# Optimization experiments

Measured on AMD Instinct MI355X. Metric: run time of the kernel, lower is better.

The kernel has to match this reference:

```python
import jax, jax.numpy as jnp
import numpy as np

N_QUBITS = 5
N_A = 1
N_LAYERS = 4
PATCH = 2 ** (N_QUBITS - N_A)  # 16

CNOT4 = jnp.array([[1, 0, 0, 0], [0, 1, 0, 0], [0, 0, 0, 1], [0, 0, 1, 0]], dtype=jnp.complex64)


def _ry(t):
    c = jnp.cos(t / 2).astype(jnp.complex64)
    s = jnp.sin(t / 2).astype(jnp.complex64)
    return jnp.stack([jnp.stack([c, -s]), jnp.stack([s, c])])


def _rot(phi, theta, omega):
    # PennyLane Rot = RZ(omega) RY(theta) RZ(phi)
    c = jnp.cos(theta / 2)
    s = jnp.sin(theta / 2)
    ep = jnp.exp(-0.5j * (phi + omega))  # e^{-i(phi+omega)/2}
    em = jnp.exp(-0.5j * (phi - omega))  # e^{-i(phi-omega)/2}
    return jnp.stack([jnp.stack([ep * c, -jnp.conj(em) * s]),
                      jnp.stack([em * s, jnp.conj(ep) * c])])


def _apply_1q(state, U, w):
    # contract U onto qubit axis w of state [2]*5
    s = jnp.tensordot(U, state, axes=(1, w))
    return jnp.moveaxis(s, 0, w)


def _apply_cnot(state, c, t):
    perm = jnp.moveaxis(state, (c, t), (0, 1))
    shp = perm.shape
    out = (CNOT4 @ perm.reshape(4, -1)).reshape(shp)
    return jnp.moveaxis(out, (0, 1), (c, t))


def _simulate(noise, w):
    # noise: [5], w: [4,5,3] -> normalized probs over first 16 basis states
    state = jnp.zeros((2,) * N_QUBITS, jnp.complex64).at[(0,) * N_QUBITS].set(1.0)
    for q in range(N_QUBITS):
        state = _apply_1q(state, _ry(noise[q]), q)
    for l in range(N_LAYERS):
        r = l % (N_QUBITS - 1) + 1  # StronglyEntanglingLayers default ranges
        for q in range(N_QUBITS):
            state = _apply_1q(state, _rot(w[l, q, 0], w[l, q, 1], w[l, q, 2]), q)
        for q in range(N_QUBITS):
            state = _apply_cnot(state, q, (q + r) % N_QUBITS)
    probs = jnp.abs(state.reshape(-1)) ** 2  # [32]
    p0 = probs[:PATCH] / jnp.sum(probs)  # partial measure: ancilla wire 4 == 0
    return p0 / jnp.max(p0)


def setup_inputs() -> dict:
    key = jax.random.key(0)
    k1, k2 = jax.random.split(key)
    B, G = 65536, 4
    x = jax.random.uniform(k1, (B, N_QUBITS), dtype=jnp.float32)
    weights = jax.random.uniform(k2, (G, N_LAYERS, N_QUBITS, 3), dtype=jnp.float32)  # q_delta=1
    return {"x": x, "weights": weights}


def reference(x, weights):
    sim_g = jax.vmap(_simulate, in_axes=(None, 0))   # over generators
    sim_bg = jax.vmap(sim_g, in_axes=(0, None))      # over batch
    out = sim_bg(x, weights)                         # [B, G, 16]
    return out.reshape(x.shape[0], -1).astype(jnp.float32)  # [B, G*16]
```

## Files before the change

kernel.cpp:

```cpp
#include <hip/hip_runtime.h>


#define NGEN 4
#define NLAY 4
#define NQ   5

typedef _Float16 half8 __attribute__((ext_vector_type(8)));
typedef float    f32x4 __attribute__((ext_vector_type(4)));

__global__ __launch_bounds__(256) void pqg_precompute(
    const float* __restrict__ w, _Float16* __restrict__ wsA)
{
    __shared__ float gm[NLAY * NQ * 8];
    __shared__ float Sr[32 * 32];
    __shared__ float Si[32 * 32];

    const int g = blockIdx.x;
    const int t = threadIdx.x;

    if (t < NLAY * NQ) {
        const float* wp = w + (g * (NLAY * NQ) + t) * 3;
        const float phi = wp[0], theta = wp[1], omega = wp[2];
        const float a = 0.5f * (phi + omega);
        const float bb = 0.5f * (phi - omega);
        const float h = 0.5f * theta;
        const float sa = __sinf(a), ca = __cosf(a);
        const float sb = __sinf(bb), cb = __cosf(bb);
        const float st = __sinf(h), ct = __cosf(h);
        float* m = &gm[t * 8];
        m[0] =  ca * ct;  m[1] = -sa * ct;
        m[2] = -cb * st;  m[3] = -sb * st;
        m[4] =  cb * st;  m[5] = -sb * st;
        m[6] =  ca * ct;  m[7] =  sa * ct;
    }

#pragma unroll
    for (int r = 0; r < 4; ++r) {
        const int idx = r * 256 + t;
        Sr[idx] = ((idx >> 5) == (idx & 31)) ? 1.0f : 0.0f;
        Si[idx] = 0.0f;
    }
    __syncthreads();

    const int col = t & 31;
    const int p0  = t >> 5;

    int gate = 0;
#pragma clang loop unroll(disable)
    for (int l = 0; l < NLAY; ++l) {
#pragma clang loop unroll(disable)
        for (int q = 0; q < NQ; ++q, ++gate) {
            const float* m = &gm[gate * 8];
            const float u00r = m[0], u00i = m[1], u01r = m[2], u01i = m[3];
            const float u10r = m[4], u10i = m[5], u11r = m[6], u11i = m[7];
            const int sb = 16 >> q;
            const int lowm = sb - 1;
#pragma unroll
            for (int r = 0; r < 2; ++r) {
                const int p = p0 + r * 8;
                const int i = ((p & ~lowm) << 1) | (p & lowm);
                const int j = i | sb;
                const int ii = i * 32 + col, jj2 = j * 32 + col;
                const float ar = Sr[ii], ai = Si[ii];
                const float br = Sr[jj2], bi = Si[jj2];
                Sr[ii] = u00r * ar - u00i * ai + u01r * br - u01i * bi;
                Si[ii] = u00r * ai + u00i * ar + u01r * bi + u01i * br;
                Sr[jj2] = u10r * ar - u10i * ai + u11r * br - u11i * bi;
                Si[jj2] = u10r * ai + u10i * ar + u11r * bi + u11i * br;
            }
            __syncthreads();
        }

        const int rr = l + 1;
        float tr[4], ti[4];
#pragma unroll
        for (int r = 0; r < 4; ++r) {
            const int idx = r * 256 + t;
            const int amp = idx >> 5;
            const int cc  = idx & 31;
            int v = amp;
#pragma unroll
            for (int q = 4; q >= 0; --q) {
                const int cb2 = 16 >> q;
                int tq = q + rr; if (tq >= NQ) tq -= NQ;
                const int tb2 = 16 >> tq;
                if (v & cb2) v ^= tb2;
            }
            tr[r] = Sr[v * 32 + cc];
            ti[r] = Si[v * 32 + cc];
        }
        __syncthreads();
#pragma unroll
        for (int r = 0; r < 4; ++r) {
            const int idx = r * 256 + t;
            Sr[idx] = tr[r];
            Si[idx] = ti[r];
        }
        __syncthreads();
    }

#pragma unroll
    for (int r = 0; r < 4; ++r) {
        const int idx = r * 256 + t;
        const int plane = idx >> 9;
        const int e = idx & 511;
        const int row = e >> 5;
        const int cc  = e & 31;
        const int L = (cc >> 3) * 16 + row;
        const int jj = cc & 7;
        const float val = plane ? Si[row * 32 + cc] : Sr[row * 32 + cc];
        wsA[((g * 2 + plane) * 64 + L) * 8 + jj] = (_Float16)val;
    }
}

#define TPB 2

__global__ __launch_bounds__(256) void pqg_main(
    const float* __restrict__ x,
    const _Float16* __restrict__ wsA,
    float* __restrict__ out)
{
    const int lane = threadIdx.x & 63;
    const int g = threadIdx.x >> 6;
    const int quad = lane >> 4;
    const int n = lane & 15;

    const half8 Ar = *(const half8*)(wsA + ((g * 2 + 0) * 64 + lane) * 8);
    const half8 Ai = *(const half8*)(wsA + ((g * 2 + 1) * 64 + lane) * 8);

    const int b_block = blockIdx.x * (16 * TPB);

#pragma unroll
    for (int t = 0; t < TPB; ++t) {
        const int b = b_block + t * 16 + n;
        const float* xb = x + b * NQ;

        float c[5], s[5];
#pragma unroll
        for (int q = 0; q < 5; ++q) {
            const float tt = 0.5f * xb[q];
            s[q] = __sinf(tt);
            c[q] = __cosf(tt);
        }

        const float f01 = ((quad & 2) ? s[0] : c[0]) * ((quad & 1) ? s[1] : c[1]);
        const float a0 = f01 * c[2], a1 = f01 * s[2];
        const float b00 = a0 * c[3], b01 = a0 * s[3];
        const float b10 = a1 * c[3], b11 = a1 * s[3];

        half8 Bf;
        Bf[0] = (_Float16)(b00 * c[4]);  Bf[1] = (_Float16)(b00 * s[4]);
        Bf[2] = (_Float16)(b01 * c[4]);  Bf[3] = (_Float16)(b01 * s[4]);
        Bf[4] = (_Float16)(b10 * c[4]);  Bf[5] = (_Float16)(b10 * s[4]);
        Bf[6] = (_Float16)(b11 * c[4]);  Bf[7] = (_Float16)(b11 * s[4]);

        f32x4 accR = {0.f, 0.f, 0.f, 0.f};
        f32x4 accI = {0.f, 0.f, 0.f, 0.f};
        accR = __builtin_amdgcn_mfma_f32_16x16x32_f16(Ar, Bf, accR, 0, 0, 0);
        accI = __builtin_amdgcn_mfma_f32_16x16x32_f16(Ai, Bf, accI, 0, 0, 0);

        float p0 = accR[0] * accR[0] + accI[0] * accI[0];
        float p1 = accR[1] * accR[1] + accI[1] * accI[1];
        float p2 = accR[2] * accR[2] + accI[2] * accI[2];
        float p3 = accR[3] * accR[3] + accI[3] * accI[3];

        float mx = fmaxf(fmaxf(p0, p1), fmaxf(p2, p3));
        mx = fmaxf(mx, __shfl_xor(mx, 16));
        mx = fmaxf(mx, __shfl_xor(mx, 32));
        const float inv = 1.0f / mx;

        float4 o = make_float4(p0 * inv, p1 * inv, p2 * inv, p3 * inv);
        *(float4*)(out + (size_t)b * 64 + g * 16 + quad * 4) = o;
    }
}

extern "C" void kernel_launch(void* const* d_in, const int* in_sizes, int n_in,
                              void* d_out, int out_size, void* d_ws, size_t ws_size,
                              hipStream_t stream) {
    const float* x = (const float*)d_in[0];
    const float* w = (const float*)d_in[1];
    float* out = (float*)d_out;
    _Float16* wsA = (_Float16*)d_ws;

    const int B = in_sizes[0] / NQ;

    pqg_precompute<<<NGEN, 256, 0, stream>>>(w, wsA);
    pqg_main<<<B / (16 * TPB), 256, 0, stream>>>(x, wsA, out);
}
```

Baseline: 72.35 us.

## Share per-sample trig and input-vector build across generators via LDS; split precompute

The main kernel previously had each of the four generator waves recompute sin/cos of all five inputs and build the product-state vector redundantly. Now 160 threads compute the trig once per block into shared memory, 256 threads build the 32-element half-precision input vectors into padded LDS, and each wave loads its MFMA B-fragment from there. The precompute kernel is also split into two 64-thread blocks per generator, each handling half of the unitary's columns with padded LDS rows. This adds two block barriers and LDS traffic in exchange for removing duplicated transcendental and scalar work.

```diff
diff --git a/kernel.cpp b/kernel.cpp
--- a/kernel.cpp
+++ b/kernel.cpp
@@ -6,17 +6,19 @@
 #define NQ   5
 
 typedef _Float16 half8 __attribute__((ext_vector_type(8)));
+typedef _Float16 half4 __attribute__((ext_vector_type(4)));
 typedef float    f32x4 __attribute__((ext_vector_type(4)));
 
-__global__ __launch_bounds__(256) void pqg_precompute(
+__global__ __launch_bounds__(64) void pqg_precompute(
     const float* __restrict__ w, _Float16* __restrict__ wsA)
 {
     __shared__ float gm[NLAY * NQ * 8];
-    __shared__ float Sr[32 * 32];
-    __shared__ float Si[32 * 32];
-
-    const int g = blockIdx.x;
-    const int t = threadIdx.x;
+    __shared__ float Sr[32 * 17];
+    __shared__ float Si[32 * 17];
+
+    const int g  = blockIdx.x >> 1;
+    const int ch = blockIdx.x & 1;
+    const int t  = threadIdx.x;
 
     if (t < NLAY * NQ) {
         const float* wp = w + (g * (NLAY * NQ) + t) * 3;
@@ -35,15 +37,17 @@
     }
 
 #pragma unroll
-    for (int r = 0; r < 4; ++r) {
-        const int idx = r * 256 + t;
-        Sr[idx] = ((idx >> 5) == (idx & 31)) ? 1.0f : 0.0f;
-        Si[idx] = 0.0f;
+    for (int r = 0; r < 8; ++r) {
+        const int idx = r * 64 + t;
+        const int amp = idx >> 4;
+        const int cL  = idx & 15;
+        Sr[amp * 17 + cL] = (amp == ch * 16 + cL) ? 1.0f : 0.0f;
+        Si[amp * 17 + cL] = 0.0f;
     }
     __syncthreads();
 
-    const int col = t & 31;
-    const int p0  = t >> 5;
+    const int colL = t & 15;
+    const int pg   = t >> 4;
 
     int gate = 0;
 #pragma clang loop unroll(disable)
@@ -56,28 +60,28 @@
             const int sb = 16 >> q;
             const int lowm = sb - 1;
 #pragma unroll
-            for (int r = 0; r < 2; ++r) {
-                const int p = p0 + r * 8;
+            for (int r = 0; r < 4; ++r) {
+                const int p = r * 4 + pg;
                 const int i = ((p & ~lowm) << 1) | (p & lowm);
                 const int j = i | sb;
-                const int ii = i * 32 + col, jj2 = j * 32 + col;
+                const int ii = i * 17 + colL, jj = j * 17 + colL;
                 const float ar = Sr[ii], ai = Si[ii];
-                const float br = Sr[jj2], bi = Si[jj2];
+                const float br = Sr[jj], bi = Si[jj];
                 Sr[ii] = u00r * ar - u00i * ai + u01r * br - u01i * bi;
                 Si[ii] = u00r * ai + u00i * ar + u01r * bi + u01i * br;
-                Sr[jj2] = u10r * ar - u10i * ai + u11r * br - u11i * bi;
-                Si[jj2] = u10r * ai + u10i * ar + u11r * bi + u11i * br;
+                Sr[jj] = u10r * ar - u10i * ai + u11r * br - u11i * bi;
+                Si[jj] = u10r * ai + u10i * ar + u11r * bi + u11i * br;
             }
             __syncthreads();
         }
 
         const int rr = l + 1;
-        float tr[4], ti[4];
-#pragma unroll
-        for (int r = 0; r < 4; ++r) {
-            const int idx = r * 256 + t;
-            const int amp = idx >> 5;
-            const int cc  = idx & 31;
+        float tr[8], ti[8];
+#pragma unroll
+        for (int r = 0; r < 8; ++r) {
+            const int idx = r * 64 + t;
+            const int amp = idx >> 4;
+            const int cc  = idx & 15;
             int v = amp;
 #pragma unroll
             for (int q = 4; q >= 0; --q) {
@@ -86,29 +90,30 @@
                 const int tb2 = 16 >> tq;
                 if (v & cb2) v ^= tb2;
             }
-            tr[r] = Sr[v * 32 + cc];
-            ti[r] = Si[v * 32 + cc];
+            tr[r] = Sr[v * 17 + cc];
+            ti[r] = Si[v * 17 + cc];
         }
         __syncthreads();
 #pragma unroll
-        for (int r = 0; r < 4; ++r) {
-            const int idx = r * 256 + t;
-            Sr[idx] = tr[r];
-            Si[idx] = ti[r];
+        for (int r = 0; r < 8; ++r) {
+            const int idx = r * 64 + t;
+            Sr[(idx >> 4) * 17 + (idx & 15)] = tr[r];
+            Si[(idx >> 4) * 17 + (idx & 15)] = ti[r];
         }
         __syncthreads();
     }
 
 #pragma unroll
-    for (int r = 0; r < 4; ++r) {
-        const int idx = r * 256 + t;
-        const int plane = idx >> 9;
-        const int e = idx & 511;
-        const int row = e >> 5;
-        const int cc  = e & 31;
-        const int L = (cc >> 3) * 16 + row;
-        const int jj = cc & 7;
-        const float val = plane ? Si[row * 32 + cc] : Sr[row * 32 + cc];
+    for (int r = 0; r < 8; ++r) {
+        const int idx = r * 64 + t;
+        const int plane = idx >> 8;
+        const int e = idx & 255;
+        const int row = e >> 4;
+        const int cL  = e & 15;
+        const int col = ch * 16 + cL;
+        const int L = (col >> 3) * 16 + row;
+        const int jj = col & 7;
+        const float val = plane ? Si[row * 17 + cL] : Sr[row * 17 + cL];
         wsA[((g * 2 + plane) * 64 + L) * 8 + jj] = (_Float16)val;
     }
 }
@@ -120,56 +125,69 @@
     const _Float16* __restrict__ wsA,
     float* __restrict__ out)
 {
-    const int lane = threadIdx.x & 63;
-    const int g = threadIdx.x >> 6;
+    __shared__ float scC[160];
+    __shared__ float scS[160];
+    __shared__ __align__(16) _Float16 vf[32 * 40];
+
+    const int tid = threadIdx.x;
+    const int lane = tid & 63;
+    const int g = tid >> 6;
     const int quad = lane >> 4;
     const int n = lane & 15;
+    const int b0 = blockIdx.x * 32;
 
     const half8 Ar = *(const half8*)(wsA + ((g * 2 + 0) * 64 + lane) * 8);
     const half8 Ai = *(const half8*)(wsA + ((g * 2 + 1) * 64 + lane) * 8);
 
-    const int b_block = blockIdx.x * (16 * TPB);
+    if (tid < 160) {
+        const float tt = 0.5f * x[b0 * 5 + tid];
+        scS[tid] = __sinf(tt);
+        scC[tid] = __cosf(tt);
+    }
+    __syncthreads();
+
+    {
+        const int bl = tid >> 3;
+        const int kq = tid & 7;
+        const float* C = &scC[bl * 5];
+        const float* S = &scS[bl * 5];
+        const float t0 = (kq & 4) ? S[0] : C[0];
+        const float t1 = (kq & 2) ? S[1] : C[1];
+        const float t2 = (kq & 1) ? S[2] : C[2];
+        const float p = t0 * t1 * t2;
+        const float pc3 = p * C[3], ps3 = p * S[3];
+        half4 hv;
+        hv[0] = (_Float16)(pc3 * C[4]);
+        hv[1] = (_Float16)(pc3 * S[4]);
+        hv[2] = (_Float16)(ps3 * C[4]);
+        hv[3] = (_Float16)(ps3 * S[4]);
+        *(half4*)(vf + bl * 40 + kq * 4) = hv;
+    }
+    __syncthreads();
 
 #pragma unroll
     for (int t = 0; t < TPB; ++t) {
-        const int b = b_block + t * 16 + n;
-        const float* xb = x + b * NQ;
-
-        float c[5], s[5];
-#pragma unroll
-        for (int q = 0; q < 5; ++q) {
-            const float tt = 0.5f * xb[q];
-            s[q] = __sinf(tt);
-            c[q] = __cosf(tt);
-        }
-
-        const float f01 = ((quad & 2) ? s[0] : c[0]) * ((quad & 1) ? s[1] : c[1]);
-        const float a0 = f01 * c[2], a1 = f01 * s[2];
-        const float b00 = a0 * c[3], b01 = a0 * s[3];
-        const float b10 = a1 * c[3], b11 = a1 * s[3];
-
-        half8 Bf;
-        Bf[0] = (_Float16)(b00 * c[4]);  Bf[1] = (_Float16)(b00 * s[4]);
-        Bf[2] = (_Float16)(b01 * c[4]);  Bf[3] = (_Float16)(b01 * s[4]);
-        Bf[4] = (_Float16)(b10 * c[4]);  Bf[5] = (_Float16)(b10 * s[4]);
-        Bf[6] = (_Float16)(b11 * c[4]);  Bf[7] = (_Float16)(b11 * s[4]);
+        const int bl = t * 16 + n;
+        const int b = b0 + bl;
+
+        const half8 Bf = *(const half8*)(vf + bl * 40 + quad * 8);
 
         f32x4 accR = {0.f, 0.f, 0.f, 0.f};
         f32x4 accI = {0.f, 0.f, 0.f, 0.f};
         accR = __builtin_amdgcn_mfma_f32_16x16x32_f16(Ar, Bf, accR, 0, 0, 0);
         accI = __builtin_amdgcn_mfma_f32_16x16x32_f16(Ai, Bf, accI, 0, 0, 0);
 
-        float p0 = accR[0] * accR[0] + accI[0] * accI[0];
-        float p1 = accR[1] * accR[1] + accI[1] * accI[1];
-        float p2 = accR[2] * accR[2] + accI[2] * accI[2];
-        float p3 = accR[3] * accR[3] + accI[3] * accI[3];
+        const float p0 = accR[0] * accR[0] + accI[0] * accI[0];
+        const float p1 = accR[1] * accR[1] + accI[1] * accI[1];
+        const float p2 = accR[2] * accR[2] + accI[2] * accI[2];
+        const float p3 = accR[3] * accR[3] + accI[3] * accI[3];
 
         float mx = fmaxf(fmaxf(p0, p1), fmaxf(p2, p3));
         mx = fmaxf(mx, __shfl_xor(mx, 16));
         mx = fmaxf(mx, __shfl_xor(mx, 32));
         const float inv = 1.0f / mx;
 
-        float4 o = make_float4(p0 * inv, p1 * inv, p2 * inv, p3 * inv);
+        const float4 o = make_float4(p0 * inv, p1 * inv, p2 * inv, p3 * inv);
         *(float4*)(out + (size_t)b * 64 + g * 16 + quad * 4) = o;
     }
 }
@@ -184,6 +202,6 @@
 
     const int B = in_sizes[0] / NQ;
 
-    pqg_precompute<<<NGEN, 256, 0, stream>>>(w, wsA);
-    pqg_main<<<B / (16 * TPB), 256, 0, stream>>>(x, wsA, out);
+    pqg_precompute<<<NGEN * 2, 64, 0, stream>>>(w, wsA);
+    pqg_main<<<B / 32, 256, 0, stream>>>(x, wsA, out);
 }
```

Result: no change. 73.47 us (+1.5%).
